# Kernel optimization log

Measured on AMD Instinct MI355X. Metric: run time of the kernel, lower is better.

## Reference

```python
import jax, jax.numpy as jnp
import numpy as np

PAD_IDX = 0

def _gru_layer(xs, W_ih, W_hh, b_ih, b_hh):
    # xs: [B, S, D]; W_ih: [3H, D]; W_hh: [3H, H]
    B = xs.shape[0]
    H = W_hh.shape[1]
    # precompute input-side gate projections for all timesteps: [S, B, 3H]
    xg = jnp.einsum('bsd,gd->sbg', xs, W_ih) + b_ih

    def step(h, xg_t):
        hg = h @ W_hh.T + b_hh                      # [B, 3H]
        xr, xz, xn = jnp.split(xg_t, 3, axis=-1)
        hr, hz, hn = jnp.split(hg, 3, axis=-1)
        r = jax.nn.sigmoid(xr + hr)
        z = jax.nn.sigmoid(xz + hz)
        n = jnp.tanh(xn + r * hn)
        h_new = (1.0 - z) * n + z * h
        return h_new, h_new

    h0 = jnp.zeros((B, H), dtype=xs.dtype)
    _, ys = jax.lax.scan(step, h0, xg)              # ys: [S, B, H]
    return jnp.transpose(ys, (1, 0, 2))             # [B, S, H]

def setup_inputs() -> dict:
    key = jax.random.key(0)
    ks = jax.random.split(key, 12)
    V, E, H = 32000, 256, 512
    B, S = 64, 512
    s_e = 1.0 / np.sqrt(H)
    inp = {
        'x': jax.random.randint(ks[0], (B, S), 0, V, dtype=jnp.int32),
        'emb': jax.random.normal(ks[1], (V, E), dtype=jnp.float32),
        'W_ih0': jax.random.uniform(ks[2], (3 * H, E), jnp.float32, -s_e, s_e),
        'W_hh0': jax.random.uniform(ks[3], (3 * H, H), jnp.float32, -s_e, s_e),
        'b_ih0': jax.random.uniform(ks[4], (3 * H,), jnp.float32, -s_e, s_e),
        'b_hh0': jax.random.uniform(ks[5], (3 * H,), jnp.float32, -s_e, s_e),
        'W_ih1': jax.random.uniform(ks[6], (3 * H, H), jnp.float32, -s_e, s_e),
        'W_hh1': jax.random.uniform(ks[7], (3 * H, H), jnp.float32, -s_e, s_e),
        'b_ih1': jax.random.uniform(ks[8], (3 * H,), jnp.float32, -s_e, s_e),
        'b_hh1': jax.random.uniform(ks[9], (3 * H,), jnp.float32, -s_e, s_e),
        'W_fc': jax.random.uniform(ks[10], (1, H), jnp.float32, -s_e, s_e),
        'b_fc': jax.random.uniform(ks[11], (1,), jnp.float32, -s_e, s_e),
    }
    return inp

def reference(x, emb, W_ih0, W_hh0, b_ih0, b_hh0, W_ih1, W_hh1, b_ih1, b_hh1, W_fc, b_fc):
    # embedding with padding_idx: pad row is zero
    emb_z = emb.at[PAD_IDX].set(0.0)
    h = emb_z[x]                                    # [B, S, E]
    h = _gru_layer(h, W_ih0, W_hh0, b_ih0, b_hh0)   # [B, S, H]
    h = _gru_layer(h, W_ih1, W_hh1, b_ih1, b_hh1)   # [B, S, H]
    final = h[:, -1, :]                             # [B, H]
    return jax.nn.sigmoid(final @ W_fc.T + b_fc)    # [B, 1]
```

## Files before the change

### kernel.cpp

```cpp
#include <hip/hip_runtime.h>
#include <math.h>

typedef short  s8v __attribute__((ext_vector_type(8)));
typedef float  f4v __attribute__((ext_vector_type(4)));
typedef unsigned long long ull;

#define S_LEN 512
#define BATCH 64
#define HID   512
#define TPB   256

#define WI0H_OFF 0L
#define WI0L_OFF 786432L
#define WH0H_OFF 1572864L
#define WH0L_OFF 3145728L
#define WI1H_OFF 4718592L
#define WI1L_OFF 6291456L
#define WH1H_OFF 7864320L
#define WH1L_OFF 9437184L
#define XEB_OFF  11010048L
#define H0R_OFF  27787264L
#define H1R_OFF  94896128L
#define NEED_FAST 95420416L

#define BAR_BYTES   4096
#define HBUF_BYTES  (HID*BATCH*4)
#define A_OFF       BAR_BYTES
#define B_OFF       (A_OFF + 2*HBUF_BYTES)
#define XE_OFF      (B_OFF + 2*HBUF_BYTES)
#define XE_BYTES    ((size_t)S_LEN*64*BATCH*16)

__device__ __forceinline__ float fexp2(float x){ return __builtin_amdgcn_exp2f(x); }
__device__ __forceinline__ float frcp (float x){ return __builtin_amdgcn_rcpf(x); }
__device__ __forceinline__ float sigm (float x){ return frcp(1.f + fexp2(-1.44269504089f*x)); }
__device__ __forceinline__ float tanhx(float x){ return 1.f - 2.f*frcp(1.f + fexp2(2.88539008178f*x)); }
__device__ __forceinline__ float sigmoid_f(float v){ return 1.0f/(1.0f + expf(-v)); }

__device__ __forceinline__ unsigned short f2bf(float f){
  unsigned int u = __float_as_uint(f);
  u = u + 0x7FFFu + ((u >> 16) & 1u);
  return (unsigned short)(u >> 16);
}
__device__ __forceinline__ float bf2f(unsigned short s){
  return __uint_as_float(((unsigned int)s) << 16);
}

__global__ void wcvt_kernel(const float* __restrict__ Wih0, const float* __restrict__ Whh0,
                            const float* __restrict__ Wih1, const float* __restrict__ Whh1,
                            char* __restrict__ ws)
{
  int idx = blockIdx.x * TPB + threadIdx.x;
  const float* src; long hi_off, lo_off; int pos;
  if (idx < 393216)       { src = Wih0; pos = idx;           hi_off = WI0H_OFF; lo_off = WI0L_OFF; }
  else if (idx < 1179648) { src = Whh0; pos = idx - 393216;  hi_off = WH0H_OFF; lo_off = WH0L_OFF; }
  else if (idx < 1966080) { src = Wih1; pos = idx - 1179648; hi_off = WI1H_OFF; lo_off = WI1L_OFF; }
  else                    { src = Whh1; pos = idx - 1966080; hi_off = WH1H_OFF; lo_off = WH1L_OFF; }
  float w = src[pos];
  unsigned short h = f2bf(w);
  unsigned short l = f2bf(w - bf2f(h));
  ((unsigned short*)(ws + hi_off))[pos] = h;
  ((unsigned short*)(ws + lo_off))[pos] = l;
}

__global__ void gather_xe_bf_kernel(const int* __restrict__ x,
                                    const float* __restrict__ emb,
                                    char* __restrict__ ws)
{
  int idx = blockIdx.x * TPB + threadIdx.x;
  int k4 = idx & 63;
  int n  = idx >> 6;
  int t = n >> 6, b = n & 63;
  int tok = x[b * S_LEN + t];
  float4 v = make_float4(0.f,0.f,0.f,0.f);
  if (tok != 0) v = ((const float4*)emb)[(size_t)tok * 64 + k4];
  unsigned int lo = (unsigned int)f2bf(v.x) | ((unsigned int)f2bf(v.y) << 16);
  unsigned int hi = (unsigned int)f2bf(v.z) | ((unsigned int)f2bf(v.w) << 16);
  ((uint2*)(ws + XEB_OFF))[(long)n * 64 + k4] = make_uint2(lo, hi);
}

__device__ __forceinline__ void st_rec(ull* p, ull v){
  __hip_atomic_store(p, v, __ATOMIC_RELAXED, __HIP_MEMORY_SCOPE_AGENT);
}

template<int NKS>
__device__ __forceinline__ void load2(const ull* __restrict__ sl, int b0, int col,
                                      int quad, int k0s, unsigned want,
                                      s8v bf[2][NKS])
{
  ull d[2][NKS][4];
  for (;;){
    #pragma unroll
    for (int ct = 0; ct < 2; ++ct){
      const int b = b0 + ct*16 + col;
      #pragma unroll
      for (int ks = 0; ks < NKS; ++ks){
        const int e = k0s + ks*4 + quad;
        const ull* p = sl + (long)(4*e)*64 + b;
        #pragma unroll
        for (int i = 0; i < 4; ++i)
          d[ct][ks][i] = __hip_atomic_load(p + (long)i*64, __ATOMIC_RELAXED, __HIP_MEMORY_SCOPE_AGENT);
      }
    }
    bool ok = true;
    #pragma unroll
    for (int ct = 0; ct < 2; ++ct)
      #pragma unroll
      for (int ks = 0; ks < NKS; ++ks)
        #pragma unroll
        for (int i = 0; i < 4; ++i)
          ok = ok && ((unsigned)(d[ct][ks][i] >> 32) == want);
    if (__all(ok)) break;
    __builtin_amdgcn_s_sleep(1);
  }
  #pragma unroll
  for (int ct = 0; ct < 2; ++ct)
    #pragma unroll
    for (int ks = 0; ks < NKS; ++ks){
      s8v v;
      #pragma unroll
      for (int i = 0; i < 4; ++i){
        unsigned lo = (unsigned)d[ct][ks][i];
        v[2*i]   = (short)(lo & 0xFFFFu);
        v[2*i+1] = (short)(lo >> 16);
      }
      bf[ct][ks] = v;
    }
}

template<int NKSI, int TAGIN>
__device__ __forceinline__ void scan_fused(
    int rowWG, int wave, int lane, int j0, int b0,
    const s8v* __restrict__ WHhi, const s8v* __restrict__ WHlo,
    const s8v* __restrict__ WIhi, const s8v* __restrict__ WIlo,
    const s8v* __restrict__ xsrc,
    const ull* __restrict__ rin,  int inSlotMask,
    const ull* __restrict__ rhid, int hidSlotMask,
    const float* __restrict__ bih, const float* __restrict__ bhh,
    ull* __restrict__ rout, int outMask,
    f4v* __restrict__ part)
{
  const int quad = lane >> 4, col = lane & 15;
  const int k0h  = wave * 16;
  const int k0i  = wave * (NKSI * 4);
  const int AKsI = TAGIN ? 64 : 32;

  s8v hh[3][4], hl[3][4], ih[3][NKSI], il[3][NKSI];
  #pragma unroll
  for (int g = 0; g < 3; ++g){
    const int row = g*512 + j0 + col;
    #pragma unroll
    for (int ks = 0; ks < 4; ++ks){
      const int e = row*64 + k0h + ks*4 + quad;
      hh[g][ks] = WHhi[e]; hl[g][ks] = WHlo[e];
    }
    #pragma unroll
    for (int ks = 0; ks < NKSI; ++ks){
      const int e = row*AKsI + k0i + ks*4 + quad;
      ih[g][ks] = WIhi[e]; il[g][ks] = WIlo[e];
    }
  }

  float cr[4], cz[4], cnx[4], cnh[4], hp[4];
  #pragma unroll
  for (int r4 = 0; r4 < 4; ++r4){
    int j = j0 + wave*4 + r4;
    cr[r4]  = bih[j]      + bhh[j];
    cz[r4]  = bih[512+j]  + bhh[512+j];
    cnx[r4] = bih[1024+j];
    cnh[r4] = bhh[1024+j];
    hp[r4]  = 0.f;
  }

  for (int t = 0; t < S_LEN; ++t){
    f4v aR[2], aZ[2], aNX[2], aNH[2];
    #pragma unroll
    for (int ct = 0; ct < 2; ++ct){
      aR[ct] = (f4v)0.f; aZ[ct] = (f4v)0.f; aNX[ct] = (f4v)0.f; aNH[ct] = (f4v)0.f;
    }

    if (TAGIN == 0){
      #pragma unroll
      for (int ct = 0; ct < 2; ++ct){
        const int nG = b0 + ct*16 + col;
        const long base = ((long)t*64 + nG)*32 + k0i + quad;
        #pragma unroll
        for (int ks = 0; ks < NKSI; ++ks){
          s8v bf = xsrc[base + ks*4];
          aR[ct]  = __builtin_amdgcn_mfma_f32_16x16x32_bf16(ih[0][ks], bf, aR[ct], 0, 0, 0);
          aR[ct]  = __builtin_amdgcn_mfma_f32_16x16x32_bf16(il[0][ks], bf, aR[ct], 0, 0, 0);
          aZ[ct]  = __builtin_amdgcn_mfma_f32_16x16x32_bf16(ih[1][ks], bf, aZ[ct], 0, 0, 0);
          aZ[ct]  = __builtin_amdgcn_mfma_f32_16x16x32_bf16(il[1][ks], bf, aZ[ct], 0, 0, 0);
          aNX[ct] = __builtin_amdgcn_mfma_f32_16x16x32_bf16(ih[2][ks], bf, aNX[ct], 0, 0, 0);
          aNX[ct] = __builtin_amdgcn_mfma_f32_16x16x32_bf16(il[2][ks], bf, aNX[ct], 0, 0, 0);
        }
      }
    } else {
      const ull* sl = rin + (long)(t & inSlotMask)*16384;
      s8v bfi[2][NKSI];
      load2<NKSI>(sl, b0, col, quad, k0i, (unsigned)(t+1), bfi);
      #pragma unroll
      for (int ct = 0; ct < 2; ++ct)
        #pragma unroll
        for (int ks = 0; ks < NKSI; ++ks){
          aR[ct]  = __builtin_amdgcn_mfma_f32_16x16x32_bf16(ih[0][ks], bfi[ct][ks], aR[ct], 0, 0, 0);
          aR[ct]  = __builtin_amdgcn_mfma_f32_16x16x32_bf16(il[0][ks], bfi[ct][ks], aR[ct], 0, 0, 0);
          aZ[ct]  = __builtin_amdgcn_mfma_f32_16x16x32_bf16(ih[1][ks], bfi[ct][ks], aZ[ct], 0, 0, 0);
          aZ[ct]  = __builtin_amdgcn_mfma_f32_16x16x32_bf16(il[1][ks], bfi[ct][ks], aZ[ct], 0, 0, 0);
          aNX[ct] = __builtin_amdgcn_mfma_f32_16x16x32_bf16(ih[2][ks], bfi[ct][ks], aNX[ct], 0, 0, 0);
          aNX[ct] = __builtin_amdgcn_mfma_f32_16x16x32_bf16(il[2][ks], bfi[ct][ks], aNX[ct], 0, 0, 0);
        }
    }

    if (t > 0){
      const ull* sl = rhid + (long)((t-1) & hidSlotMask)*16384;
      s8v bfh[2][4];
      load2<4>(sl, b0, col, quad, k0h, (unsigned)t, bfh);
      #pragma unroll
      for (int ct = 0; ct < 2; ++ct)
        #pragma unroll
        for (int ks = 0; ks < 4; ++ks){
          aR[ct]  = __builtin_amdgcn_mfma_f32_16x16x32_bf16(hh[0][ks], bfh[ct][ks], aR[ct], 0, 0, 0);
          aR[ct]  = __builtin_amdgcn_mfma_f32_16x16x32_bf16(hl[0][ks], bfh[ct][ks], aR[ct], 0, 0, 0);
          aZ[ct]  = __builtin_amdgcn_mfma_f32_16x16x32_bf16(hh[1][ks], bfh[ct][ks], aZ[ct], 0, 0, 0);
          aZ[ct]  = __builtin_amdgcn_mfma_f32_16x16x32_bf16(hl[1][ks], bfh[ct][ks], aZ[ct], 0, 0, 0);
          aNH[ct] = __builtin_amdgcn_mfma_f32_16x16x32_bf16(hh[2][ks], bfh[ct][ks], aNH[ct], 0, 0, 0);
          aNH[ct] = __builtin_amdgcn_mfma_f32_16x16x32_bf16(hl[2][ks], bfh[ct][ks], aNH[ct], 0, 0, 0);
        }
    }

    f4v* pb = part + (t & 1)*2048;
    #pragma unroll
    for (int ct = 0; ct < 2; ++ct){
      pb[((wave*4 + 0)*2 + ct)*64 + lane] = aR[ct];
      pb[((wave*4 + 1)*2 + ct)*64 + lane] = aZ[ct];
      pb[((wave*4 + 2)*2 + ct)*64 + lane] = aNX[ct];
      pb[((wave*4 + 3)*2 + ct)*64 + lane] = aNH[ct];
    }

    asm volatile("s_waitcnt lgkmcnt(0)" ::: "memory");
    __builtin_amdgcn_s_barrier();
    asm volatile("" ::: "memory");

    if (lane < 32){
      const int b = lane;
      const int ct = b >> 4;
      const int pl = wave*16 + (b & 15);
      f4v sr = (f4v)0.f, sz = (f4v)0.f, snx = (f4v)0.f, snh = (f4v)0.f;
      #pragma unroll
      for (int sw = 0; sw < 4; ++sw){
        sr  += pb[((sw*4 + 0)*2 + ct)*64 + pl];
        sz  += pb[((sw*4 + 1)*2 + ct)*64 + pl];
        snx += pb[((sw*4 + 2)*2 + ct)*64 + pl];
        snh += pb[((sw*4 + 3)*2 + ct)*64 + pl];
      }
      const int slotw = t & outMask;
      const ull tg = ((ull)(unsigned)(t + 1)) << 32;
      ull* ob = rout + (long)slotw*16384 + (long)(rowWG*8 + wave*2)*64 + (b0 + b);
      #pragma unroll
      for (int pr = 0; pr < 2; ++pr){
        unsigned short h2[2];
        #pragma unroll
        for (int q = 0; q < 2; ++q){
          const int r4 = pr*2 + q;
          float r = sigm(sr[r4] + cr[r4]);
          float z = sigm(sz[r4] + cz[r4]);
          float n = tanhx(snx[r4] + cnx[r4] + r*(snh[r4] + cnh[r4]));
          float h = n + z*(hp[r4] - n);
          hp[r4] = h;
          h2[q] = f2bf(h);
        }
        st_rec(ob + pr*64, ((ull)((unsigned)h2[0] | ((unsigned)h2[1] << 16))) | tg);
      }
    }
  }
}

__global__ __launch_bounds__(TPB, 1) void gru_mfma_kernel(
    const float* __restrict__ bih0, const float* __restrict__ bhh0,
    const float* __restrict__ bih1, const float* __restrict__ bhh1,
    const float* __restrict__ Wfc,  const float* __restrict__ bfc,
    float* __restrict__ out, char* __restrict__ ws)
{
  __shared__ f4v part[2*2048];

  const int tid  = threadIdx.x;
  const int wg   = blockIdx.x;
  const int lane = tid & 63;
  const int wave = tid >> 6;
  const int isL1 = (wg >= 64);
  const int lw   = wg & 63;
  const int rowWG = lw >> 1;
  const int bh    = lw & 1;
  const int j0 = rowWG * 16;
  const int b0 = bh * 32;

  const s8v* wi0h = (const s8v*)(ws + WI0H_OFF); const s8v* wi0l = (const s8v*)(ws + WI0L_OFF);
  const s8v* wh0h = (const s8v*)(ws + WH0H_OFF); const s8v* wh0l = (const s8v*)(ws + WH0L_OFF);
  const s8v* wi1h = (const s8v*)(ws + WI1H_OFF); const s8v* wi1l = (const s8v*)(ws + WI1L_OFF);
  const s8v* wh1h = (const s8v*)(ws + WH1H_OFF); const s8v* wh1l = (const s8v*)(ws + WH1L_OFF);
  const s8v* xeb = (const s8v*)(ws + XEB_OFF);
  const ull* h0r = (const ull*)(ws + H0R_OFF);
  const ull* h1r = (const ull*)(ws + H1R_OFF);
  ull* h0w = (ull*)(ws + H0R_OFF);
  ull* h1w = (ull*)(ws + H1R_OFF);

  if (!isL1){
    scan_fused<2,0>(rowWG, wave, lane, j0, b0,
                    wh0h, wh0l, wi0h, wi0l, xeb,
                    h0r, 0, h0r, 0x3FFFFFFF,
                    bih0, bhh0, h0w, 0x3FFFFFFF, part);
  } else {
    scan_fused<4,1>(rowWG, wave, lane, j0, b0,
                    wh1h, wh1l, wi1h, wi1l, xeb,
                    h0r, 0x3FFFFFFF, h1r, 3,
                    bih1, bhh1, h1w, 3, part);
  }

  if (wg == 64 && wave == 0){
    const ull* sl = h1r + 3L*16384;
    float acc = bfc[0];
    for (int c0 = 0; c0 < 256; c0 += 32){
      ull d[32];
      for (;;){
        #pragma unroll
        for (int i = 0; i < 32; ++i)
          d[i] = __hip_atomic_load(sl + (long)(c0+i)*64 + lane,
                                   __ATOMIC_RELAXED, __HIP_MEMORY_SCOPE_AGENT);
        bool ok = true;
        #pragma unroll
        for (int i = 0; i < 32; ++i) ok = ok && ((unsigned)(d[i] >> 32) == 512u);
        if (__all(ok)) break;
        __builtin_amdgcn_s_sleep(1);
      }
      #pragma unroll
      for (int i = 0; i < 32; ++i){
        unsigned lo = (unsigned)d[i];
        int u = (c0 + i) * 2;
        acc += bf2f((unsigned short)(lo & 0xFFFFu)) * Wfc[u]
             + bf2f((unsigned short)(lo >> 16))     * Wfc[u+1];
      }
    }
    out[lane] = sigm(acc);
  }
}

__global__ void gather_xe_kernel(const int* __restrict__ x,
                                 const float* __restrict__ emb,
                                 float4* __restrict__ xe4)
{
  int idx = blockIdx.x * TPB + threadIdx.x;
  int b  = idx & 63;
  int k4 = (idx >> 6) & 63;
  int t  = idx >> 12;
  int tok = x[b * S_LEN + t];
  float4 v = make_float4(0.f, 0.f, 0.f, 0.f);
  if (tok != 0) v = ((const float4*)emb)[(size_t)tok * 64 + k4];
  xe4[idx] = v;
}

__device__ __forceinline__ void accum_vec(const float4* __restrict__ xin,
                                          const float4* __restrict__ w0,
                                          const float4* __restrict__ w1,
                                          const float4* __restrict__ w2,
                                          int n4, int lane,
                                          float& ar, float& az, float& an)
{
  #pragma unroll 4
  for (int k = 0; k < n4; ++k){
    float4 xv = xin[k * 64 + lane];
    float4 wr = w0[k], wz = w1[k], wn = w2[k];
    ar = fmaf(xv.x, wr.x, ar); az = fmaf(xv.x, wz.x, az); an = fmaf(xv.x, wn.x, an);
    ar = fmaf(xv.y, wr.y, ar); az = fmaf(xv.y, wz.y, az); an = fmaf(xv.y, wn.y, an);
    ar = fmaf(xv.z, wr.z, ar); az = fmaf(xv.z, wz.z, az); an = fmaf(xv.z, wn.z, an);
    ar = fmaf(xv.w, wr.w, ar); az = fmaf(xv.w, wz.w, az); an = fmaf(xv.w, wn.w, an);
  }
}

__device__ __forceinline__ void accum_emb(const int* __restrict__ x,
                                          const float* __restrict__ emb, int t,
                                          const float4* __restrict__ w0,
                                          const float4* __restrict__ w1,
                                          const float4* __restrict__ w2,
                                          int lane, float& ar, float& az, float& an)
{
  int tok = x[lane * S_LEN + t];
  const float4* erow = (const float4*)emb + (size_t)tok * 64;
  float m = (tok != 0) ? 1.0f : 0.0f;
  #pragma unroll 4
  for (int k = 0; k < 64; ++k){
    float4 xv = erow[k];
    float xx = xv.x*m, xy = xv.y*m, xz = xv.z*m, xw = xv.w*m;
    float4 wr = w0[k], wz = w1[k], wn = w2[k];
    ar = fmaf(xx, wr.x, ar); az = fmaf(xx, wz.x, az); an = fmaf(xx, wn.x, an);
    ar = fmaf(xy, wr.y, ar); az = fmaf(xy, wz.y, az); an = fmaf(xy, wn.y, an);
    ar = fmaf(xz, wr.z, ar); az = fmaf(xz, wz.z, az); an = fmaf(xz, wn.z, an);
    ar = fmaf(xw, wr.w, ar); az = fmaf(xw, wz.w, az); an = fmaf(xw, wn.w, an);
  }
}

__device__ __forceinline__ void stage_weights(float4* wlds, int tid, int j0, int kin4,
                                              const float* Wih, const float* Whh)
{
  const int per = 3 * (kin4 + 128);
  for (int idx = tid; idx < 4 * per; idx += TPB){
    int w = idx / per, rem = idx - w * per;
    int g = rem / (kin4 + 128), k = rem - g * (kin4 + 128);
    int row = g * HID + j0 + w;
    float4 v;
    if (k < kin4) v = ((const float4*)Wih)[(size_t)row * kin4 + k];
    else          v = ((const float4*)Whh)[(size_t)row * 128 + (k - kin4)];
    wlds[(w * 3 + g) * 256 + k] = v;
  }
}

__device__ __forceinline__ void barrier_tick(int* bar, int wg, int tid, int phase)
{
  __syncthreads();
  if (tid == 0){
    __builtin_amdgcn_fence(__ATOMIC_RELEASE, "agent");
    int* leaf = bar + 32 + (wg >> 4) * 32;
    int old = __hip_atomic_fetch_add(leaf, 1, __ATOMIC_ACQ_REL, __HIP_MEMORY_SCOPE_AGENT);
    if (old == phase * 16 + 15){
      __hip_atomic_fetch_add(bar, 1, __ATOMIC_ACQ_REL, __HIP_MEMORY_SCOPE_AGENT);
    }
    const int target = (phase + 1) * 16;
    while (__hip_atomic_load(bar, __ATOMIC_ACQUIRE, __HIP_MEMORY_SCOPE_AGENT) < target){
      __builtin_amdgcn_s_sleep(2);
    }
    __builtin_amdgcn_fence(__ATOMIC_ACQUIRE, "agent");
  }
  __syncthreads();
}

__device__ __forceinline__ void finish_store(const float4* __restrict__ hprev,
                                             float ar, float az, float anx, float anh,
                                             int lane, int j, float4* __restrict__ hout)
{
  float r  = sigmoid_f(ar);
  float zz = sigmoid_f(az);
  float n  = tanhf(fmaf(r, anh, anx));
  int fi = ((j >> 2) * 64 + lane) * 4 + (j & 3);
  float hhp = ((const float*)hprev)[fi];
  ((float*)hout)[fi] = fmaf(zz, hhp - n, n);
}

__global__ __launch_bounds__(TPB) void gru_persist_kernel(
    const int*   __restrict__ x,    const float* __restrict__ emb,
    const float* __restrict__ Wih0, const float* __restrict__ Whh0,
    const float* __restrict__ bih0, const float* __restrict__ bhh0,
    const float* __restrict__ Wih1, const float* __restrict__ Whh1,
    const float* __restrict__ bih1, const float* __restrict__ bhh1,
    const float* __restrict__ Wfc,  const float* __restrict__ bfc,
    float* __restrict__ out, int* __restrict__ bar,
    float4* __restrict__ A0, float4* __restrict__ A1,
    float4* __restrict__ B0, float4* __restrict__ B1,
    const float4* __restrict__ xe4, int use_xe)
{
  __shared__ float4 wlds[3072];
  const int tid  = threadIdx.x;
  const int wg   = blockIdx.x;
  const int lane = tid & 63;
  const int wave = tid >> 6;
  const bool isL1 = (wg >= 128);
  const int j0   = (isL1 ? wg - 128 : wg) * 4;
  const int kin4 = isL1 ? 128 : 64;

  stage_weights(wlds, tid, j0, kin4, isL1 ? Wih1 : Wih0, isL1 ? Whh1 : Whh0);
  __syncthreads();

  const int j = j0 + wave;
  const float* bih = isL1 ? bih1 : bih0;
  const float* bhh = isL1 ? bhh1 : bhh0;
  const float br  = bih[j]        + bhh[j];
  const float bz  = bih[j + 512]  + bhh[j + 512];
  const float bnx = bih[j + 1024];
  const float bnh = bhh[j + 1024];

  const float4* w0 = &wlds[(wave * 3 + 0) * 256];
  const float4* w1 = &wlds[(wave * 3 + 1) * 256];
  const float4* w2 = &wlds[(wave * 3 + 2) * 256];

  float4* A[2] = {A0, A1};
  float4* B[2] = {B0, B1};

  for (int t = 0; t <= S_LEN; ++t){
    if (!isL1){
      if (t < S_LEN){
        const float4* hprev = A[(t + 1) & 1];
        float ar = br, az = bz, anx = bnx, anh = bnh;
        if (use_xe) accum_vec(xe4 + (size_t)t * 4096, w0, w1, w2, 64, lane, ar, az, anx);
        else        accum_emb(x, emb, t, w0, w1, w2, lane, ar, az, anx);
        accum_vec(hprev, w0 + 64, w1 + 64, w2 + 64, 128, lane, ar, az, anh);
        finish_store(hprev, ar, az, anx, anh, lane, j, A[t & 1]);
      }
    } else if (t >= 1){
      const int u = t - 1;
      const float4* xin   = A[u & 1];
      const float4* hprev = B[(u + 1) & 1];
      float ar = br, az = bz, anx = bnx, anh = bnh;
      accum_vec(xin,   w0,       w1,       w2,       128, lane, ar, az, anx);
      accum_vec(hprev, w0 + 128, w1 + 128, w2 + 128, 128, lane, ar, az, anh);
      finish_store(hprev, ar, az, anx, anh, lane, j, B[u & 1]);
    }
    barrier_tick(bar, wg, tid, t);
  }

  if (wg == 0 && wave == 0){
    float acc = bfc[0];
    const float4* h1 = B[1];
    const float4* wf = (const float4*)Wfc;
    #pragma unroll 4
    for (int k = 0; k < 128; ++k){
      float4 hv = h1[k * 64 + lane];
      float4 wv = wf[k];
      acc = fmaf(hv.x, wv.x, acc); acc = fmaf(hv.y, wv.y, acc);
      acc = fmaf(hv.z, wv.z, acc); acc = fmaf(hv.w, wv.w, acc);
    }
    out[lane] = sigmoid_f(acc);
  }
}

extern "C" void kernel_launch(void* const* d_in, const int* in_sizes, int n_in,
                              void* d_out, int out_size, void* d_ws, size_t ws_size,
                              hipStream_t stream)
{
  (void)in_sizes; (void)n_in; (void)out_size;
  const int*   x    = (const int*)  d_in[0];
  const float* emb  = (const float*)d_in[1];
  const float* Wih0 = (const float*)d_in[2];
  const float* Whh0 = (const float*)d_in[3];
  const float* bih0 = (const float*)d_in[4];
  const float* bhh0 = (const float*)d_in[5];
  const float* Wih1 = (const float*)d_in[6];
  const float* Whh1 = (const float*)d_in[7];
  const float* bih1 = (const float*)d_in[8];
  const float* bhh1 = (const float*)d_in[9];
  const float* Wfc  = (const float*)d_in[10];
  const float* bfc  = (const float*)d_in[11];
  float* out = (float*)d_out;
  char* ws = (char*)d_ws;

  if (ws_size >= (size_t)NEED_FAST){
    wcvt_kernel<<<2752512 / TPB, TPB, 0, stream>>>(Wih0, Whh0, Wih1, Whh1, ws);
    gather_xe_bf_kernel<<<2097152 / TPB, TPB, 0, stream>>>(x, emb, ws);
    gru_mfma_kernel<<<128, TPB, 0, stream>>>(bih0, bhh0, bih1, bhh1, Wfc, bfc, out, ws);
  } else {
    int*    bar = (int*)ws;
    float4* A0  = (float4*)(ws + A_OFF);
    float4* A1  = (float4*)(ws + A_OFF + HBUF_BYTES);
    float4* B0  = (float4*)(ws + B_OFF);
    float4* B1  = (float4*)(ws + B_OFF + HBUF_BYTES);
    float4* xe4 = (float4*)(ws + XE_OFF);
    const int use_xe = (ws_size >= (size_t)XE_OFF + XE_BYTES) ? 1 : 0;
    hipMemsetAsync(ws, 0, XE_OFF, stream);
    if (use_xe){
      gather_xe_kernel<<<(S_LEN * 64 * BATCH) / TPB, TPB, 0, stream>>>(x, emb, xe4);
    }
    gru_persist_kernel<<<256, TPB, 0, stream>>>(
        x, emb, Wih0, Whh0, bih0, bhh0, Wih1, Whh1, bih1, bhh1, Wfc, bfc,
        out, bar, A0, A1, B0, B1, xe4, use_xe);
  }
}
```

Before: 2.095 ms.

## Reorder recurrent state records for contiguous loads and try plain loads first

Changes the layout of the tagged hidden-state ring buffer so each lane's four records for a k-group sit contiguously (e*256 + b*4 + i), allowing wider, coalesced reads. The hidden-state load is issued early with ordinary (non-atomic) loads, and the input and hidden loads fall back to the relaxed-atomic spin loop only when the tags are stale. The goal is to cut per-step latency on the cross-workgroup dependency chain. Plain loads may be served from a stale cache line, but the tag check guards correctness and forces the atomic retry path in that case.

```diff
diff --git a/kernel.cpp b/kernel.cpp
--- a/kernel.cpp
+++ b/kernel.cpp
@@ -83,11 +83,41 @@
 }
 
 template<int NKS>
-__device__ __forceinline__ void load2(const ull* __restrict__ sl, int b0, int col,
-                                      int quad, int k0s, unsigned want,
-                                      s8v bf[2][NKS])
-{
-  ull d[2][NKS][4];
+__device__ __forceinline__ void load_plain(const ull* __restrict__ sl, int b0, int col,
+                                           int quad, int k0s, ull d[2][NKS][4])
+{
+  #pragma unroll
+  for (int ct = 0; ct < 2; ++ct){
+    const int b = b0 + ct*16 + col;
+    #pragma unroll
+    for (int ks = 0; ks < NKS; ++ks){
+      const int e = k0s + ks*4 + quad;
+      const ull* p = sl + (long)e*256 + (long)b*4;
+      #pragma unroll
+      for (int i = 0; i < 4; ++i) d[ct][ks][i] = p[i];
+    }
+  }
+}
+
+template<int NKS>
+__device__ __forceinline__ bool tags_ok(const ull d[2][NKS][4], unsigned want)
+{
+  bool ok = true;
+  #pragma unroll
+  for (int ct = 0; ct < 2; ++ct)
+    #pragma unroll
+    for (int ks = 0; ks < NKS; ++ks)
+      #pragma unroll
+      for (int i = 0; i < 4; ++i)
+        ok = ok && ((unsigned)(d[ct][ks][i] >> 32) == want);
+  return __all(ok);
+}
+
+template<int NKS>
+__device__ __forceinline__ void load_sc1(const ull* __restrict__ sl, int b0, int col,
+                                         int quad, int k0s, unsigned want,
+                                         ull d[2][NKS][4])
+{
   for (;;){
     #pragma unroll
     for (int ct = 0; ct < 2; ++ct){
@@ -95,23 +125,20 @@
       #pragma unroll
       for (int ks = 0; ks < NKS; ++ks){
         const int e = k0s + ks*4 + quad;
-        const ull* p = sl + (long)(4*e)*64 + b;
+        const ull* p = sl + (long)e*256 + (long)b*4;
         #pragma unroll
         for (int i = 0; i < 4; ++i)
-          d[ct][ks][i] = __hip_atomic_load(p + (long)i*64, __ATOMIC_RELAXED, __HIP_MEMORY_SCOPE_AGENT);
-      }
-    }
-    bool ok = true;
-    #pragma unroll
-    for (int ct = 0; ct < 2; ++ct)
-      #pragma unroll
-      for (int ks = 0; ks < NKS; ++ks)
-        #pragma unroll
-        for (int i = 0; i < 4; ++i)
-          ok = ok && ((unsigned)(d[ct][ks][i] >> 32) == want);
-    if (__all(ok)) break;
+          d[ct][ks][i] = __hip_atomic_load(p + i, __ATOMIC_RELAXED, __HIP_MEMORY_SCOPE_AGENT);
+      }
+    }
+    if (tags_ok<NKS>(d, want)) break;
     __builtin_amdgcn_s_sleep(1);
   }
+}
+
+template<int NKS>
+__device__ __forceinline__ void unpack_recs(const ull d[2][NKS][4], s8v bf[2][NKS])
+{
   #pragma unroll
   for (int ct = 0; ct < 2; ++ct)
     #pragma unroll
@@ -177,6 +204,11 @@
     for (int ct = 0; ct < 2; ++ct){
       aR[ct] = (f4v)0.f; aZ[ct] = (f4v)0.f; aNX[ct] = (f4v)0.f; aNH[ct] = (f4v)0.f;
     }
+
+    const ull* slh = rhid + (long)((t-1) & hidSlotMask)*16384;
+    const unsigned wanth = (unsigned)t;
+    ull hd[2][4][4];
+    if (t > 0) load_plain<4>(slh, b0, col, quad, k0h, hd);
 
     if (TAGIN == 0){
       #pragma unroll
@@ -195,9 +227,14 @@
         }
       }
     } else {
-      const ull* sl = rin + (long)(t & inSlotMask)*16384;
+      const ull* sli = rin + (long)(t & inSlotMask)*16384;
+      const unsigned wanti = (unsigned)(t+1);
+      ull idt[2][NKSI][4];
+      load_plain<NKSI>(sli, b0, col, quad, k0i, idt);
+      if (!tags_ok<NKSI>(idt, wanti))
+        load_sc1<NKSI>(sli, b0, col, quad, k0i, wanti, idt);
       s8v bfi[2][NKSI];
-      load2<NKSI>(sl, b0, col, quad, k0i, (unsigned)(t+1), bfi);
+      unpack_recs<NKSI>(idt, bfi);
       #pragma unroll
       for (int ct = 0; ct < 2; ++ct)
         #pragma unroll
@@ -212,9 +249,10 @@
     }
 
     if (t > 0){
-      const ull* sl = rhid + (long)((t-1) & hidSlotMask)*16384;
+      if (!tags_ok<4>(hd, wanth))
+        load_sc1<4>(slh, b0, col, quad, k0h, wanth, hd);
       s8v bfh[2][4];
-      load2<4>(sl, b0, col, quad, k0h, (unsigned)t, bfh);
+      unpack_recs<4>(hd, bfh);
       #pragma unroll
       for (int ct = 0; ct < 2; ++ct)
         #pragma unroll
@@ -255,7 +293,9 @@
       }
       const int slotw = t & outMask;
       const ull tg = ((ull)(unsigned)(t + 1)) << 32;
-      ull* ob = rout + (long)slotw*16384 + (long)(rowWG*8 + wave*2)*64 + (b0 + b);
+      ull* ob = rout + (long)slotw*16384
+                     + (long)(rowWG*2 + (wave>>1))*256
+                     + (long)(b0 + b)*4 + (wave&1)*2;
       #pragma unroll
       for (int pr = 0; pr < 2; ++pr){
         unsigned short h2[2];
@@ -269,7 +309,7 @@
           hp[r4] = h;
           h2[q] = f2bf(h);
         }
-        st_rec(ob + pr*64, ((ull)((unsigned)h2[0] | ((unsigned)h2[1] << 16))) | tg);
+        st_rec(ob + pr, ((ull)((unsigned)h2[0] | ((unsigned)h2[1] << 16))) | tg);
       }
     }
   }
@@ -323,9 +363,11 @@
       ull d[32];
       for (;;){
         #pragma unroll
-        for (int i = 0; i < 32; ++i)
-          d[i] = __hip_atomic_load(sl + (long)(c0+i)*64 + lane,
+        for (int i = 0; i < 32; ++i){
+          const int c = c0 + i;
+          d[i] = __hip_atomic_load(sl + (long)(c >> 2)*256 + (long)lane*4 + (c & 3),
                                    __ATOMIC_RELAXED, __HIP_MEMORY_SCOPE_AGENT);
+        }
         bool ok = true;
         #pragma unroll
         for (int i = 0; i < 32; ++i) ok = ok && ((unsigned)(d[i] >> 32) == 512u);
```

Result: slower. 2.765 ms (+32.0%).
